# Kernel tuning notes

Hardware: AMD Instinct MI355X
Metric: run time of the kernel (lower is better)

## Reference

```python
import jax, jax.numpy as jnp
import numpy as np
from jax import lax

EPS_LN = 1e-5
EPS_NORM = 1e-12

def conv1x1(x, w):
    # x: [b,c,h,w], w: [o,c]
    return jnp.einsum('oc,bchw->bohw', w, x)

def dwconv3x3(x, w):
    # depthwise 3x3, w: [c,1,3,3]
    return lax.conv_general_dilated(
        x, w, window_strides=(1, 1), padding=[(1, 1), (1, 1)],
        feature_group_count=x.shape[1],
        dimension_numbers=('NCHW', 'OIHW', 'NCHW'))

def layernorm_chan(x, w, b):
    # WithBias LayerNorm over channel dim of NCHW (torch does it in b,(hw),c layout)
    mu = jnp.mean(x, axis=1, keepdims=True)
    var = jnp.mean((x - mu) ** 2, axis=1, keepdims=True)
    xn = (x - mu) / jnp.sqrt(var + EPS_LN)
    return xn * w[None, :, None, None] + b[None, :, None, None]

def l2norm(x):
    n = jnp.sqrt(jnp.sum(x * x, axis=-1, keepdims=True))
    return x / jnp.maximum(n, EPS_NORM)

def setup_inputs() -> dict:
    key = jax.random.key(0)
    ks = jax.random.split(key, 8)
    dim, heads, hidden = 64, 2, 170
    b, h, w = 2, 256, 256
    s = 0.05
    return {
        'x': jax.random.normal(ks[0], (b, dim, h, w), jnp.float32),
        'ln1_w': jnp.ones((dim,), jnp.float32),
        'ln1_b': jnp.zeros((dim,), jnp.float32),
        'w_qkv': jax.random.normal(ks[1], (dim * 3, dim), jnp.float32) * s,
        'dw_qkv': jax.random.normal(ks[2], (dim * 3, 1, 3, 3), jnp.float32) * s,
        'temperature': jnp.ones((heads, 1, 1), jnp.float32),
        'w_po': jax.random.normal(ks[3], (dim, dim), jnp.float32) * s,
        'ln2_w': jnp.ones((dim,), jnp.float32),
        'ln2_b': jnp.zeros((dim,), jnp.float32),
        'w_in': jax.random.normal(ks[4], (hidden * 2, dim), jnp.float32) * s,
        'dw_ffn': jax.random.normal(ks[5], (hidden * 2, 1, 3, 3), jnp.float32) * s,
        'w_out': jax.random.normal(ks[6], (dim, hidden), jnp.float32) * s,
    }

def attention(x, w_qkv, dw_qkv, temperature, w_po, num_heads):
    b, c, h, w = x.shape
    qkv = dwconv3x3(conv1x1(x, w_qkv), dw_qkv)            # [b,3c,h,w]
    q, k, v = jnp.split(qkv, 3, axis=1)
    def heads(t):
        return t.reshape(b, num_heads, c // num_heads, h * w)  # [b,hd,ch,hw]
    q, k, v = heads(q), heads(k), heads(v)
    q = l2norm(q)
    k = l2norm(k)
    attn = jnp.einsum('bhcs,bhds->bhcd', q, k) * temperature[None]  # [b,hd,ch,ch]
    attn = jax.nn.softmax(attn, axis=-1)
    out = jnp.einsum('bhcd,bhds->bhcs', attn, v)
    out = out.reshape(b, c, h, w)
    return conv1x1(out, w_po)

def gdfn(x, w_in, dw_ffn, w_out):
    x = dwconv3x3(conv1x1(x, w_in), dw_ffn)
    x1, x2 = jnp.split(x, 2, axis=1)
    return conv1x1(jax.nn.gelu(x1, approximate=False) * x2, w_out)

def reference(x, ln1_w, ln1_b, w_qkv, dw_qkv, temperature, w_po,
              ln2_w, ln2_b, w_in, dw_ffn, w_out):
    num_heads = temperature.shape[0]
    x = x + attention(layernorm_chan(x, ln1_w, ln1_b), w_qkv, dw_qkv,
                      temperature, w_po, num_heads)
    x = x + gdfn(layernorm_chan(x, ln2_w, ln2_b), w_in, dw_ffn, w_out)
    return x
```

## Files before the change

### kernel.cpp

```cpp
#include <hip/hip_runtime.h>
#include <math.h>

#define HW 65536

typedef __attribute__((ext_vector_type(8))) short short8;
typedef __attribute__((ext_vector_type(4))) float floatx4;
typedef __attribute__((ext_vector_type(4))) unsigned short ushortx4;

__device__ __forceinline__ float bf2f(unsigned short u){
  unsigned v = ((unsigned)u)<<16; float f; __builtin_memcpy(&f,&v,4); return f;
}
__device__ __forceinline__ unsigned short f2bf(float f){
  unsigned u; __builtin_memcpy(&u,&f,4);
  u += 0x7fffu + ((u>>16)&1u);
  return (unsigned short)(u>>16);
}
__device__ __forceinline__ int is_f32(const void* magic){
  return ((const unsigned*)magic)[0] == 0x3F800000u;
}
__device__ __forceinline__ float ldv(const void* p, size_t i, int f32){
  return f32 ? ((const float*)p)[i] : bf2f(((const unsigned short*)p)[i]);
}

__global__ __launch_bounds__(64) void k_fold(const void* __restrict__ w_qkv,
                       const void* __restrict__ ln1_w,
                       const void* __restrict__ ln1_b,
                       const void* __restrict__ w_in,
                       const void* __restrict__ ln2_w,
                       const void* __restrict__ ln2_b,
                       const void* __restrict__ w_out,
                       unsigned short* __restrict__ A1, float* __restrict__ a1, float* __restrict__ b1,
                       unsigned short* __restrict__ A5, float* __restrict__ a5, float* __restrict__ b5,
                       unsigned short* __restrict__ A7){
  int f32 = is_f32(ln1_w);
  int bid = blockIdx.x; int c = threadIdx.x;
  if (bid < 192){
    int j = bid;
    float wv = ldv(w_qkv, j*64+c, f32);
    unsigned short q = f2bf(wv*ldv(ln1_w,c,f32));
    A1[j*64+c] = q;
    float sa = bf2f(q);
    float sb = wv*ldv(ln1_b,c,f32);
    #pragma unroll
    for(int o=1;o<64;o<<=1){ sa += __shfl_xor(sa,o,64); sb += __shfl_xor(sb,o,64); }
    if (c==0){ a1[j]=sa; b1[j]=sb; }
  } else if (bid < 576){
    int j = bid-192;
    float wv = (j<340)? ldv(w_in, j*64+c, f32) : 0.f;
    unsigned short q = f2bf(wv*ldv(ln2_w,c,f32));
    A5[j*64+c]=q;
    float sa = bf2f(q);
    float sb = wv*ldv(ln2_b,c,f32);
    #pragma unroll
    for(int o=1;o<64;o<<=1){ sa += __shfl_xor(sa,o,64); sb += __shfl_xor(sb,o,64); }
    if (c==0){ a5[j]=sa; b5[j]=sb; }
  } else {
    int j = bid-576;
    #pragma unroll
    for(int t=0;t<3;t++){
      int k=t*64+c;
      A7[j*192+k] = (k<170)? f2bf(ldv(w_out, j*170+k, f32)) : (unsigned short)0;
    }
  }
}

#define BTT_STR 72
template<int F32>
__device__ __forceinline__ void gemm_ln_body(
    const unsigned short* __restrict__ A, const void* __restrict__ Bv,
    const float* __restrict__ arow, const float* __restrict__ brow,
    unsigned short* __restrict__ out, int outC, int jmax, int ntiles)
{
  __shared__ unsigned short btt[64*BTT_STR];
  __shared__ float muL[64];
  __shared__ float rsL[64];
  int tid=threadIdx.x; int w=tid>>6, lane=tid&63, m=lane&15, quad=lane>>4;
  int sblk = blockIdx.x*64; int b=sblk>>16, s=sblk&65535;
  {
    int ch = lane, px0 = w*16;
    size_t src = (size_t)b*64*HW + (size_t)ch*HW + s + px0;
    unsigned short tmp[16];
    if (F32){
      const float* sp = (const float*)Bv + src;
      #pragma unroll
      for(int q4=0;q4<4;q4++){
        floatx4 fv = *(const floatx4*)(sp + q4*4);
        #pragma unroll
        for(int k=0;k<4;k++) tmp[q4*4+k] = f2bf(fv[k]);
      }
    } else {
      const unsigned short* sp = (const unsigned short*)Bv + src;
      short8 r0 = *(const short8*)sp;
      short8 r1 = *(const short8*)(sp+8);
      #pragma unroll
      for(int jj=0;jj<8;jj++){ tmp[jj]=(unsigned short)r0[jj]; tmp[8+jj]=(unsigned short)r1[jj]; }
    }
    #pragma unroll
    for(int jj=0;jj<16;jj++) btt[(px0+jj)*BTT_STR + ch] = tmp[jj];
  }
  __syncthreads();
  short8 bfr[4][2];
  #pragma unroll
  for(int st4=0; st4<4; st4++){
    const unsigned short* row = btt + (st4*16+m)*BTT_STR + quad*8;
    short8 v0 = *(const short8*)row;
    short8 v1 = *(const short8*)(row+32);
    bfr[st4][0]=v0; bfr[st4][1]=v1;
    float sm=0.f, sq=0.f;
    #pragma unroll
    for(int jj=0;jj<8;jj++){
      float a=bf2f((unsigned short)v0[jj]); sm+=a; sq+=a*a;
      float c=bf2f((unsigned short)v1[jj]); sm+=c; sq+=c*c;
    }
    sm += __shfl_xor(sm,16,64); sq += __shfl_xor(sq,16,64);
    sm += __shfl_xor(sm,32,64); sq += __shfl_xor(sq,32,64);
    float m_ = sm*(1.f/64.f);
    float var = sq*(1.f/64.f) - m_*m_;
    if (w==0 && quad==0){ muL[st4*16+m]=m_; rsL[st4*16+m]=1.f/sqrtf(var+1e-5f); }
  }
  __syncthreads();
  for(int jt=w; jt<ntiles; jt+=4){
    int j = jt*16 + m;
    const unsigned short* ap = A + j*64 + quad*8;
    short8 af0 = *(const short8*)ap;
    short8 af1 = *(const short8*)(ap+32);
    float aj = arow[j], bj = brow[j];
    unsigned short* op = out + ((size_t)b*outC + j)*HW + s;
    bool ok = (j < jmax);
    #pragma unroll
    for(int st4=0; st4<4; st4++){
      floatx4 acc = {0.f,0.f,0.f,0.f};
      acc = __builtin_amdgcn_mfma_f32_16x16x32_bf16(bfr[st4][0], af0, acc, 0,0,0);
      acc = __builtin_amdgcn_mfma_f32_16x16x32_bf16(bfr[st4][1], af1, acc, 0,0,0);
      floatx4 m4 = *(const floatx4*)(muL + st4*16 + quad*4);
      floatx4 r4 = *(const floatx4*)(rsL + st4*16 + quad*4);
      ushortx4 pk;
      #pragma unroll
      for(int r=0;r<4;r++) pk[r] = f2bf(r4[r]*(acc[r] - m4[r]*aj) + bj);
      if (ok) *(ushortx4*)(op + st4*16 + quad*4) = pk;
    }
  }
}
__global__ __launch_bounds__(256) void k_gemm_ln(
    const unsigned short* __restrict__ A, const void* __restrict__ B,
    const float* __restrict__ arow, const float* __restrict__ brow,
    unsigned short* __restrict__ out,
    int outC, int jmax, int ntiles, const void* __restrict__ magic, int mode)
{
  int f32 = (mode==1) ? 1 : (mode==2 ? 0 : is_f32(magic));
  if (f32) gemm_ln_body<1>(A,B,arow,brow,out,outC,jmax,ntiles);
  else     gemm_ln_body<0>(A,B,arow,brow,out,outC,jmax,ntiles);
}

#define GTT_STR 200
__global__ __launch_bounds__(256) void k_gemm_out(
    const unsigned short* __restrict__ A7, const unsigned short* __restrict__ G,
    const unsigned short* __restrict__ xmid, void* __restrict__ outp, const void* __restrict__ magic)
{
  __shared__ unsigned short gtt[64*GTT_STR];
  int f32 = is_f32(magic);
  int tid=threadIdx.x; int w=tid>>6, lane=tid&63, m=lane&15, quad=lane>>4;
  int sblk = blockIdx.x*64; int b=sblk>>16, s=sblk&65535;
  const unsigned short* Gb = G + (size_t)b*170*HW + s;
  {
    int px0 = w*16;
    #pragma unroll
    for(int rep=0; rep<3; rep++){
      int ch = rep*64 + lane;
      const unsigned short* sp = Gb + (size_t)ch*HW + px0;
      short8 r0 = *(const short8*)sp;
      short8 r1 = *(const short8*)(sp+8);
      #pragma unroll
      for(int jj=0;jj<8;jj++){
        gtt[(px0+jj)*GTT_STR + ch]   = (unsigned short)r0[jj];
        gtt[(px0+8+jj)*GTT_STR + ch] = (unsigned short)r1[jj];
      }
    }
  }
  __syncthreads();
  int j = w*16 + m;
  const unsigned short* ap = A7 + j*192 + quad*8;
  short8 af[6];
  #pragma unroll
  for(int ks=0;ks<6;ks++) af[ks] = *(const short8*)(ap + ks*32);
  #pragma unroll
  for(int st4=0; st4<4; st4++){
    const unsigned short* row = gtt + (st4*16+m)*GTT_STR + quad*8;
    floatx4 acc = {0.f,0.f,0.f,0.f};
    #pragma unroll
    for(int ks=0;ks<6;ks++){
      short8 bf = *(const short8*)(row + ks*32);
      acc = __builtin_amdgcn_mfma_f32_16x16x32_bf16(bf, af[ks], acc, 0,0,0);
    }
    size_t idx0 = ((size_t)b*64 + j)*HW + s + st4*16 + quad*4;
    ushortx4 xm4 = *(const ushortx4*)(xmid + idx0);
    if (f32){
      floatx4 o;
      #pragma unroll
      for(int r=0;r<4;r++) o[r] = acc[r] + bf2f(xm4[r]);
      *(floatx4*)((float*)outp + idx0) = o;
    } else {
      ushortx4 o;
      #pragma unroll
      for(int r=0;r<4;r++) o[r] = f2bf(acc[r] + bf2f(xm4[r]));
      *(ushortx4*)((unsigned short*)outp + idx0) = o;
    }
  }
}

#define TSTRIDE 72
#define TROWS 66
#define TDW 34

__device__ __forceinline__ void stage_tile(unsigned short* __restrict__ tile,
    const unsigned short* __restrict__ sp, int y0, int x0, int tid){
  int ly = tid/TDW, dc = tid - ly*TDW;
  for(int i=tid; i<TROWS*TDW; i+=256){
    int gy = y0+ly-1, gx = x0+2*dc-2;
    unsigned v = 0;
    if((unsigned)gy<256u && (unsigned)gx<256u)
      v = *(const unsigned*)(sp + gy*256 + gx);
    *(unsigned*)(tile + ly*TSTRIDE + 2*dc) = v;
    ly += 7; dc += 18; if(dc>=TDW){dc-=TDW; ly++;}
  }
}

__device__ __forceinline__ void stage_tile2(unsigned short* __restrict__ t1,
    unsigned short* __restrict__ t2,
    const unsigned short* __restrict__ s1, const unsigned short* __restrict__ s2,
    int y0, int x0, int tid){
  int ly = tid/TDW, dc = tid - ly*TDW;
  for(int i=tid; i<TROWS*TDW; i+=256){
    int gy = y0+ly-1, gx = x0+2*dc-2;
    unsigned v1 = 0, v2 = 0;
    if((unsigned)gy<256u && (unsigned)gx<256u){
      int o = gy*256+gx;
      v1 = *(const unsigned*)(s1 + o);
      v2 = *(const unsigned*)(s2 + o);
    }
    *(unsigned*)(t1 + ly*TSTRIDE + 2*dc) = v1;
    *(unsigned*)(t2 + ly*TSTRIDE + 2*dc) = v2;
    ly += 7; dc += 18; if(dc>=TDW){dc-=TDW; ly++;}
  }
}

__device__ __forceinline__ void row_window(const unsigned short* __restrict__ tile,
    int ly, int tx, float* __restrict__ f){
  short8 v0 = *(const short8*)(tile + ly*TSTRIDE + 8*tx);
  short8 v1 = *(const short8*)(tile + ly*TSTRIDE + 8*tx + 8);
  #pragma unroll
  for(int k=0;k<8;k++){ f[k]=bf2f((unsigned short)v0[k]); f[k+8]=bf2f((unsigned short)v1[k]); }
}

__global__ __launch_bounds__(256) void k_dwconv(const unsigned short* __restrict__ src,
    const void* __restrict__ wdw, unsigned short* __restrict__ dst, int C,
    const void* __restrict__ magic){
  int f32 = is_f32(magic);
  __shared__ unsigned short tile[TROWS*TSTRIDE];
  int tid=threadIdx.x;
  int bc = blockIdx.y;
  int ch = bc % C;
  int t = blockIdx.x; int ty0=t>>2, tx0=t&3;
  int y0=ty0*64, x0=tx0*64;
  const unsigned short* sp = src + (size_t)bc*HW;
  stage_tile(tile, sp, y0, x0, tid);
  float w9[9];
  #pragma unroll
  for(int i=0;i<9;i++) w9[i]=ldv(wdw, ch*9+i, f32);
  __syncthreads();
  int tx=tid&7, ty=tid>>3;
  float acc0[8], acc1[8];
  #pragma unroll
  for(int i=0;i<8;i++){ acc0[i]=0.f; acc1[i]=0.f; }
  #pragma unroll
  for(int r=0;r<4;r++){
    int ly = 2*ty + r;
    float f[16];
    row_window(tile, ly, tx, f);
    #pragma unroll
    for(int yy=0;yy<2;yy++){
      int dy = r-yy;
      if (dy>=0 && dy<3){
        float* acc = yy? acc1 : acc0;
        #pragma unroll
        for(int i=0;i<8;i++)
          #pragma unroll
          for(int dx=0;dx<3;dx++)
            acc[i] += w9[dy*3+dx]*f[i+1+dx];
      }
    }
  }
  unsigned short* dp = dst + (size_t)bc*HW + (size_t)(y0+2*ty)*256 + x0 + 8*tx;
  short8 st0, st1;
  #pragma unroll
  for(int i=0;i<8;i++){ st0[i]=(short)f2bf(acc0[i]); st1[i]=(short)f2bf(acc1[i]); }
  *(short8*)dp = st0;
  *(short8*)(dp+256) = st1;
}

__global__ __launch_bounds__(256) void k_ffn_dw(const unsigned short* __restrict__ src,
    const void* __restrict__ wdw, unsigned short* __restrict__ g,
    const void* __restrict__ magic){
  int f32 = is_f32(magic);
  __shared__ unsigned short t1[TROWS*TSTRIDE];
  __shared__ unsigned short t2[TROWS*TSTRIDE];
  int tid=threadIdx.x;
  int bi = blockIdx.y;
  int b = bi/170, i = bi - b*170;
  int t = blockIdx.x; int ty0=t>>2, tx0=t&3;
  int y0=ty0*64, x0=tx0*64;
  const unsigned short* s1 = src + ((size_t)b*340 + i)*HW;
  const unsigned short* s2 = src + ((size_t)b*340 + 170 + i)*HW;
  stage_tile2(t1, t2, s1, s2, y0, x0, tid);
  float wa[9], wb[9];
  #pragma unroll
  for(int q=0;q<9;q++){ wa[q]=ldv(wdw, i*9+q, f32); wb[q]=ldv(wdw, (i+170)*9+q, f32); }
  __syncthreads();
  int tx=tid&7, ty=tid>>3;
  float a0[8], a1v[8], c0[8], c1[8];
  #pragma unroll
  for(int k=0;k<8;k++){ a0[k]=0.f; a1v[k]=0.f; c0[k]=0.f; c1[k]=0.f; }
  #pragma unroll
  for(int r=0;r<4;r++){
    int ly = 2*ty + r;
    float f[16];
    row_window(t1, ly, tx, f);
    #pragma unroll
    for(int yy=0;yy<2;yy++){
      int dy = r-yy;
      if (dy>=0 && dy<3){
        float* acc = yy? a1v : a0;
        #pragma unroll
        for(int k=0;k<8;k++)
          #pragma unroll
          for(int dx=0;dx<3;dx++)
            acc[k] += wa[dy*3+dx]*f[k+1+dx];
      }
    }
    row_window(t2, ly, tx, f);
    #pragma unroll
    for(int yy=0;yy<2;yy++){
      int dy = r-yy;
      if (dy>=0 && dy<3){
        float* acc = yy? c1 : c0;
        #pragma unroll
        for(int k=0;k<8;k++)
          #pragma unroll
          for(int dx=0;dx<3;dx++)
            acc[k] += wb[dy*3+dx]*f[k+1+dx];
      }
    }
  }
  unsigned short* gp = g + ((size_t)b*170 + i)*HW + (size_t)(y0+2*ty)*256 + x0 + 8*tx;
  short8 st0, st1;
  #pragma unroll
  for(int k=0;k<8;k++){
    float u0 = a0[k]*(1.59576912f + 0.07135481f*a0[k]*a0[k]);
    float u1 = a1v[k]*(1.59576912f + 0.07135481f*a1v[k]*a1v[k]);
    float ge0 = a0[k]/(1.f + __expf(-u0));
    float ge1 = a1v[k]/(1.f + __expf(-u1));
    st0[k]=(short)f2bf(ge0*c0[k]);
    st1[k]=(short)f2bf(ge1*c1[k]);
  }
  *(short8*)gp = st0;
  *(short8*)(gp+256) = st1;
}

__global__ __launch_bounds__(256) void k_attn_qk(const unsigned short* __restrict__ qkv,
    float* __restrict__ S, float* __restrict__ qn, float* __restrict__ kn){
  int tid=threadIdx.x; int w=tid>>6, lane=tid&63, m=lane&15, quad=lane>>4;
  int ct=w>>1, dt=w&1;
  int bh=blockIdx.y; int b=bh>>1, hd=bh&1;
  int p0 = blockIdx.x*512;
  const unsigned short* qrow = qkv + ((size_t)(b*192 + hd*32 + ct*16 + m))*HW + p0 + quad*8;
  const unsigned short* krow = qkv + ((size_t)(b*192 + 64 + hd*32 + dt*16 + m))*HW + p0 + quad*8;
  floatx4 acc = {0.f,0.f,0.f,0.f};
  float nq=0.f, nk=0.f;
  for(int it=0; it<16; it++){
    short8 a = *(const short8*)(qrow + it*32);
    short8 bq = *(const short8*)(krow + it*32);
    if (dt==0){
      #pragma unroll
      for(int jj=0;jj<8;jj++){ float v=bf2f((unsigned short)a[jj]); nq+=v*v; }
    }
    if (ct==0){
      #pragma unroll
      for(int jj=0;jj<8;jj++){ float v=bf2f((unsigned short)bq[jj]); nk+=v*v; }
    }
    acc = __builtin_amdgcn_mfma_f32_16x16x32_bf16(a, bq, acc, 0,0,0);
  }
  nq += __shfl_xor(nq,16,64); nq += __shfl_xor(nq,32,64);
  nk += __shfl_xor(nk,16,64); nk += __shfl_xor(nk,32,64);
  if (dt==0 && quad==0) atomicAdd(&qn[bh*32 + ct*16 + m], nq);
  if (ct==0 && quad==0) atomicAdd(&kn[bh*32 + dt*16 + m], nk);
  #pragma unroll
  for(int r=0;r<4;r++)
    atomicAdd(&S[(bh*32 + ct*16 + quad*4 + r)*32 + dt*16 + m], acc[r]);
}

__global__ void k_attn_fin(const float* __restrict__ S, const float* __restrict__ qn,
    const float* __restrict__ kn, const void* __restrict__ temp,
    const void* __restrict__ w_po, unsigned short* __restrict__ Mbf,
    const void* __restrict__ magic){
  int f32 = is_f32(magic);
  __shared__ float attn[2][32][32];
  __shared__ float invq[64], invk[64];
  int b = blockIdx.x; int tid=threadIdx.x;
  if (tid<64){
    int bh=b*2+(tid>>5); int c=tid&31;
    invq[tid] = 1.f/fmaxf(sqrtf(qn[bh*32+c]),1e-12f);
    invk[tid] = 1.f/fmaxf(sqrtf(kn[bh*32+c]),1e-12f);
  }
  __syncthreads();
  if (tid<64){
    int hd=tid>>5, c=tid&31; int bh=b*2+hd;
    float tmp = ldv(temp, hd, f32);
    float row[32]; float mx=-1e30f;
    for(int d=0;d<32;d++){
      float v = S[(bh*32+c)*32+d]*invq[tid]*invk[hd*32+d]*tmp;
      row[d]=v; mx=fmaxf(mx,v);
    }
    float sum=0.f;
    for(int d=0;d<32;d++){ row[d]=expf(row[d]-mx); sum+=row[d]; }
    float inv=1.f/sum;
    for(int d=0;d<32;d++) attn[hd][c][d]=row[d]*inv;
  }
  __syncthreads();
  for(int idx=tid; idx<4096; idx+=256){
    int o=idx>>6, d=idx&63; int hd=d>>5, dd=d&31;
    float sacc=0.f;
    for(int c=0;c<32;c++) sacc += ldv(w_po, o*64 + hd*32 + c, f32) * attn[hd][c][dd];
    Mbf[(size_t)b*4096 + o*64 + d] = f2bf(sacc);
  }
}

#define XSTR 72
__global__ __launch_bounds__(256) void k_attn_ffn(const void* __restrict__ x,
    const unsigned short* __restrict__ qkv, const unsigned short* __restrict__ Mbf,
    unsigned short* __restrict__ xmid,
    const unsigned short* __restrict__ A5, const float* __restrict__ a5, const float* __restrict__ b5,
    unsigned short* __restrict__ ffn_pre, const void* __restrict__ magic){
  __shared__ unsigned short vtt[64*XSTR];
  __shared__ unsigned short xt[64*XSTR];
  __shared__ float muL[64];
  __shared__ float rsL[64];
  int f32 = is_f32(magic);
  int tid=threadIdx.x; int w=tid>>6, lane=tid&63, m=lane&15, quad=lane>>4;
  int sblk = blockIdx.x*64; int b=sblk>>16, s=sblk&65535;
  const unsigned short* vp = qkv + ((size_t)(b*192 + 128))*HW + s;
  {
    int ch = lane, px0 = w*16;
    const unsigned short* sp = vp + (size_t)ch*HW + px0;
    short8 r0 = *(const short8*)sp;
    short8 r1 = *(const short8*)(sp+8);
    #pragma unroll
    for(int jj=0;jj<8;jj++){
      vtt[(px0+jj)*XSTR + ch]   = (unsigned short)r0[jj];
      vtt[(px0+8+jj)*XSTR + ch] = (unsigned short)r1[jj];
    }
  }
  int jme = w*16 + m;
  const unsigned short* ap = Mbf + (size_t)b*4096 + jme*64 + quad*8;
  short8 af0 = *(const short8*)ap;
  short8 af1 = *(const short8*)(ap+32);
  __syncthreads();
  short8 bfr[4][2];
  #pragma unroll
  for(int st4=0; st4<4; st4++){
    const unsigned short* row = vtt + (st4*16+m)*XSTR + quad*8;
    bfr[st4][0] = *(const short8*)row;
    bfr[st4][1] = *(const short8*)(row+32);
  }
  size_t xbase = (size_t)b*64*HW + s;
  #pragma unroll
  for(int st4=0; st4<4; st4++){
    floatx4 acc = {0.f,0.f,0.f,0.f};
    acc = __builtin_amdgcn_mfma_f32_16x16x32_bf16(bfr[st4][0], af0, acc, 0,0,0);
    acc = __builtin_amdgcn_mfma_f32_16x16x32_bf16(bfr[st4][1], af1, acc, 0,0,0);
    size_t idx0 = xbase + (size_t)jme*HW + st4*16 + quad*4;
    ushortx4 h;
    if (f32){
      floatx4 x4 = *(const floatx4*)((const float*)x + idx0);
      #pragma unroll
      for(int r=0;r<4;r++) h[r] = f2bf(acc[r] + x4[r]);
    } else {
      ushortx4 x4 = *(const ushortx4*)((const unsigned short*)x + idx0);
      #pragma unroll
      for(int r=0;r<4;r++) h[r] = f2bf(acc[r] + bf2f(x4[r]));
    }
    *(ushortx4*)(xmid + idx0) = h;
    #pragma unroll
    for(int r=0;r<4;r++) xt[(st4*16+quad*4+r)*XSTR + jme] = h[r];
  }
  __syncthreads();
  #pragma unroll
  for(int st4=0; st4<4; st4++){
    const unsigned short* row = xt + (st4*16+m)*XSTR + quad*8;
    short8 v0 = *(const short8*)row;
    short8 v1 = *(const short8*)(row+32);
    bfr[st4][0]=v0; bfr[st4][1]=v1;
    float sm=0.f, sq=0.f;
    #pragma unroll
    for(int jj=0;jj<8;jj++){
      float a=bf2f((unsigned short)v0[jj]); sm+=a; sq+=a*a;
      float c=bf2f((unsigned short)v1[jj]); sm+=c; sq+=c*c;
    }
    sm += __shfl_xor(sm,16,64); sq += __shfl_xor(sq,16,64);
    sm += __shfl_xor(sm,32,64); sq += __shfl_xor(sq,32,64);
    float m_ = sm*(1.f/64.f);
    float var = sq*(1.f/64.f) - m_*m_;
    if (w==0 && quad==0){ muL[st4*16+m]=m_; rsL[st4*16+m]=1.f/sqrtf(var+1e-5f); }
  }
  __syncthreads();
  for(int jt=w; jt<24; jt+=4){
    int j = jt*16 + m;
    const unsigned short* a5p = A5 + j*64 + quad*8;
    short8 g0 = *(const short8*)a5p;
    short8 g1 = *(const short8*)(a5p+32);
    float aj = a5[j], bj = b5[j];
    unsigned short* op = ffn_pre + ((size_t)b*340 + j)*HW + s;
    bool ok = (j < 340);
    #pragma unroll
    for(int st4=0; st4<4; st4++){
      floatx4 acc = {0.f,0.f,0.f,0.f};
      acc = __builtin_amdgcn_mfma_f32_16x16x32_bf16(bfr[st4][0], g0, acc, 0,0,0);
      acc = __builtin_amdgcn_mfma_f32_16x16x32_bf16(bfr[st4][1], g1, acc, 0,0,0);
      floatx4 m4 = *(const floatx4*)(muL + st4*16 + quad*4);
      floatx4 r4 = *(const floatx4*)(rsL + st4*16 + quad*4);
      ushortx4 pk;
      #pragma unroll
      for(int r=0;r<4;r++) pk[r] = f2bf(r4[r]*(acc[r] - m4[r]*aj) + bj);
      if (ok) *(ushortx4*)(op + st4*16 + quad*4) = pk;
    }
  }
}

extern "C" void kernel_launch(void* const* d_in, const int* in_sizes, int n_in,
                              void* d_out, int out_size, void* d_ws, size_t ws_size,
                              hipStream_t stream){
  (void)in_sizes; (void)n_in; (void)out_size; (void)ws_size;
  const void* x     = d_in[0];
  const void* ln1_w = d_in[1];
  const void* ln1_b = d_in[2];
  const void* w_qkv = d_in[3];
  const void* dw_qkv= d_in[4];
  const void* temp  = d_in[5];
  const void* w_po  = d_in[6];
  const void* ln2_w = d_in[7];
  const void* ln2_b = d_in[8];
  const void* w_in  = d_in[9];
  const void* dw_ffn= d_in[10];
  const void* w_out = d_in[11];

  char* ws = (char*)d_ws;
  size_t off = 0;
  auto alloc = [&](size_t n)->void*{ void* p = ws + off; off = (off + n + 255) & ~(size_t)255; return p; };

  unsigned short* A1 = (unsigned short*)alloc(192*64*2);
  float* a1 = (float*)alloc(192*4);
  float* b1 = (float*)alloc(192*4);
  unsigned short* A5 = (unsigned short*)alloc(384*64*2);
  float* a5 = (float*)alloc(384*4);
  float* b5 = (float*)alloc(384*4);
  unsigned short* A7 = (unsigned short*)alloc(64*192*2);
  float* S  = (float*)alloc(4*32*32*4);
  float* qn = (float*)alloc(128*4);
  float* kn = (float*)alloc(128*4);
  unsigned short* Mbf = (unsigned short*)alloc(2*64*64*2);
  unsigned short* xmid = (unsigned short*)alloc((size_t)2*64*HW*2);
  unsigned short* regionA = (unsigned short*)alloc((size_t)2*340*HW*2);
  unsigned short* regionB = (unsigned short*)alloc((size_t)2*192*HW*2);

  k_fold<<<dim3(640), dim3(64), 0, stream>>>(w_qkv, ln1_w, ln1_b, w_in, ln2_w, ln2_b, w_out,
                                             A1, a1, b1, A5, a5, b5, A7);

  k_gemm_ln<<<dim3(2048), dim3(256), 0, stream>>>(A1, x, a1, b1, regionA, 192, 192, 12, ln1_w, 0);
  k_dwconv<<<dim3(16,384), dim3(256), 0, stream>>>(regionA, dw_qkv, regionB, 192, ln1_w);

  hipMemsetAsync(S, 0, 16384+512+512, stream);
  k_attn_qk<<<dim3(128,4), dim3(256), 0, stream>>>(regionB, S, qn, kn);
  k_attn_fin<<<dim3(2), dim3(256), 0, stream>>>(S, qn, kn, temp, w_po, Mbf, ln1_w);

  k_attn_ffn<<<dim3(2048), dim3(256), 0, stream>>>(x, regionB, Mbf, xmid,
                                                   A5, a5, b5, regionA, ln1_w);
  k_ffn_dw<<<dim3(16,340), dim3(256), 0, stream>>>(regionA, dw_ffn, regionB, ln1_w);
  k_gemm_out<<<dim3(2048), dim3(256), 0, stream>>>(A7, regionB, xmid, d_out, ln1_w);
}
```

Measured before the change: 312.5 us.

## Replace LDS-tiled depthwise convs with register rolling-row column strips

Both depthwise 3x3 kernels drop the shared-memory halo tile and barrier. Each thread now owns an 8-pixel column strip of 16 rows and loads rows straight from global memory into a rotating 4-row register window, with halo pixels fetched as scalar loads. The grid shrinks from 16 to 2 blocks per channel. This removes LDS staging and the sync and cuts the vertical halo overhead. In exchange it adds unaligned scalar edge loads, a longer serial dependency per thread, and fewer blocks in flight.

```diff
diff --git a/kernel.cpp b/kernel.cpp
--- a/kernel.cpp
+++ b/kernel.cpp
@@ -208,162 +208,112 @@
   }
 }
 
-#define TSTRIDE 72
-#define TROWS 66
-#define TDW 34
-
-__device__ __forceinline__ void stage_tile(unsigned short* __restrict__ tile,
-    const unsigned short* __restrict__ sp, int y0, int x0, int tid){
-  int ly = tid/TDW, dc = tid - ly*TDW;
-  for(int i=tid; i<TROWS*TDW; i+=256){
-    int gy = y0+ly-1, gx = x0+2*dc-2;
-    unsigned v = 0;
-    if((unsigned)gy<256u && (unsigned)gx<256u)
-      v = *(const unsigned*)(sp + gy*256 + gx);
-    *(unsigned*)(tile + ly*TSTRIDE + 2*dc) = v;
-    ly += 7; dc += 18; if(dc>=TDW){dc-=TDW; ly++;}
-  }
-}
-
-__device__ __forceinline__ void stage_tile2(unsigned short* __restrict__ t1,
-    unsigned short* __restrict__ t2,
-    const unsigned short* __restrict__ s1, const unsigned short* __restrict__ s2,
-    int y0, int x0, int tid){
-  int ly = tid/TDW, dc = tid - ly*TDW;
-  for(int i=tid; i<TROWS*TDW; i+=256){
-    int gy = y0+ly-1, gx = x0+2*dc-2;
-    unsigned v1 = 0, v2 = 0;
-    if((unsigned)gy<256u && (unsigned)gx<256u){
-      int o = gy*256+gx;
-      v1 = *(const unsigned*)(s1 + o);
-      v2 = *(const unsigned*)(s2 + o);
-    }
-    *(unsigned*)(t1 + ly*TSTRIDE + 2*dc) = v1;
-    *(unsigned*)(t2 + ly*TSTRIDE + 2*dc) = v2;
-    ly += 7; dc += 18; if(dc>=TDW){dc-=TDW; ly++;}
-  }
-}
-
-__device__ __forceinline__ void row_window(const unsigned short* __restrict__ tile,
-    int ly, int tx, float* __restrict__ f){
-  short8 v0 = *(const short8*)(tile + ly*TSTRIDE + 8*tx);
-  short8 v1 = *(const short8*)(tile + ly*TSTRIDE + 8*tx + 8);
-  #pragma unroll
-  for(int k=0;k<8;k++){ f[k]=bf2f((unsigned short)v0[k]); f[k+8]=bf2f((unsigned short)v1[k]); }
+__device__ __forceinline__ void load_row(const unsigned short* __restrict__ sp,
+    int y, int x0, int oct, float* __restrict__ f){
+  if((unsigned)y < 256u){
+    const unsigned short* p = sp + y*256 + x0;
+    short8 v = *(const short8*)p;
+    #pragma unroll
+    for(int k=0;k<8;k++) f[k+1] = bf2f((unsigned short)v[k]);
+    f[0] = oct      ? bf2f(p[-1]) : 0.f;
+    f[9] = (oct<31) ? bf2f(p[8])  : 0.f;
+  } else {
+    #pragma unroll
+    for(int k=0;k<10;k++) f[k] = 0.f;
+  }
+}
+
+__device__ __forceinline__ void conv_row(const float* __restrict__ r0,
+    const float* __restrict__ r1, const float* __restrict__ r2,
+    const float* __restrict__ w, float* __restrict__ o){
+  #pragma unroll
+  for(int k=0;k<8;k++){
+    o[k] = w[0]*r0[k] + w[1]*r0[k+1] + w[2]*r0[k+2]
+         + w[3]*r1[k] + w[4]*r1[k+1] + w[5]*r1[k+2]
+         + w[6]*r2[k] + w[7]*r2[k+1] + w[8]*r2[k+2];
+  }
 }
 
 __global__ __launch_bounds__(256) void k_dwconv(const unsigned short* __restrict__ src,
     const void* __restrict__ wdw, unsigned short* __restrict__ dst, int C,
     const void* __restrict__ magic){
   int f32 = is_f32(magic);
-  __shared__ unsigned short tile[TROWS*TSTRIDE];
   int tid=threadIdx.x;
   int bc = blockIdx.y;
   int ch = bc % C;
-  int t = blockIdx.x; int ty0=t>>2, tx0=t&3;
-  int y0=ty0*64, x0=tx0*64;
+  int oct = tid&31, strip = tid>>5;
+  int x0 = oct*8;
+  int y0 = blockIdx.x*128 + strip*16;
   const unsigned short* sp = src + (size_t)bc*HW;
-  stage_tile(tile, sp, y0, x0, tid);
   float w9[9];
   #pragma unroll
   for(int i=0;i<9;i++) w9[i]=ldv(wdw, ch*9+i, f32);
-  __syncthreads();
-  int tx=tid&7, ty=tid>>3;
-  float acc0[8], acc1[8];
-  #pragma unroll
-  for(int i=0;i<8;i++){ acc0[i]=0.f; acc1[i]=0.f; }
-  #pragma unroll
-  for(int r=0;r<4;r++){
-    int ly = 2*ty + r;
-    float f[16];
-    row_window(tile, ly, tx, f);
-    #pragma unroll
-    for(int yy=0;yy<2;yy++){
-      int dy = r-yy;
-      if (dy>=0 && dy<3){
-        float* acc = yy? acc1 : acc0;
-        #pragma unroll
-        for(int i=0;i<8;i++)
-          #pragma unroll
-          for(int dx=0;dx<3;dx++)
-            acc[i] += w9[dy*3+dx]*f[i+1+dx];
-      }
-    }
-  }
-  unsigned short* dp = dst + (size_t)bc*HW + (size_t)(y0+2*ty)*256 + x0 + 8*tx;
-  short8 st0, st1;
-  #pragma unroll
-  for(int i=0;i<8;i++){ st0[i]=(short)f2bf(acc0[i]); st1[i]=(short)f2bf(acc1[i]); }
-  *(short8*)dp = st0;
-  *(short8*)(dp+256) = st1;
+  unsigned short* dp = dst + (size_t)bc*HW + (size_t)y0*256 + x0;
+  float A[10],B[10],C_[10],D[10];
+  load_row(sp, y0-1, x0, oct, A);
+  load_row(sp, y0,   x0, oct, B);
+  load_row(sp, y0+1, x0, oct, C_);
+  int y = y0;
+#define DSTEP(P,Q,R,S) { \
+    load_row(sp, y+2, x0, oct, S); \
+    float o8[8]; \
+    conv_row(P,Q,R, w9, o8); \
+    short8 st; \
+    _Pragma("unroll") \
+    for(int k=0;k<8;k++) st[k]=(short)f2bf(o8[k]); \
+    *(short8*)dp = st; dp += 256; y++; }
+  for(int t=0;t<4;t++){
+    DSTEP(A,B,C_,D)
+    DSTEP(B,C_,D,A)
+    DSTEP(C_,D,A,B)
+    DSTEP(D,A,B,C_)
+  }
+#undef DSTEP
 }
 
 __global__ __launch_bounds__(256) void k_ffn_dw(const unsigned short* __restrict__ src,
     const void* __restrict__ wdw, unsigned short* __restrict__ g,
     const void* __restrict__ magic){
   int f32 = is_f32(magic);
-  __shared__ unsigned short t1[TROWS*TSTRIDE];
-  __shared__ unsigned short t2[TROWS*TSTRIDE];
   int tid=threadIdx.x;
   int bi = blockIdx.y;
   int b = bi/170, i = bi - b*170;
-  int t = blockIdx.x; int ty0=t>>2, tx0=t&3;
-  int y0=ty0*64, x0=tx0*64;
+  int oct = tid&31, strip = tid>>5;
+  int x0 = oct*8;
+  int y0 = blockIdx.x*128 + strip*16;
   const unsigned short* s1 = src + ((size_t)b*340 + i)*HW;
   const unsigned short* s2 = src + ((size_t)b*340 + 170 + i)*HW;
-  stage_tile2(t1, t2, s1, s2, y0, x0, tid);
   float wa[9], wb[9];
   #pragma unroll
   for(int q=0;q<9;q++){ wa[q]=ldv(wdw, i*9+q, f32); wb[q]=ldv(wdw, (i+170)*9+q, f32); }
-  __syncthreads();
-  int tx=tid&7, ty=tid>>3;
-  float a0[8], a1v[8], c0[8], c1[8];
-  #pragma unroll
-  for(int k=0;k<8;k++){ a0[k]=0.f; a1v[k]=0.f; c0[k]=0.f; c1[k]=0.f; }
-  #pragma unroll
-  for(int r=0;r<4;r++){
-    int ly = 2*ty + r;
-    float f[16];
-    row_window(t1, ly, tx, f);
-    #pragma unroll
-    for(int yy=0;yy<2;yy++){
-      int dy = r-yy;
-      if (dy>=0 && dy<3){
-        float* acc = yy? a1v : a0;
-        #pragma unroll
-        for(int k=0;k<8;k++)
-          #pragma unroll
-          for(int dx=0;dx<3;dx++)
-            acc[k] += wa[dy*3+dx]*f[k+1+dx];
-      }
-    }
-    row_window(t2, ly, tx, f);
-    #pragma unroll
-    for(int yy=0;yy<2;yy++){
-      int dy = r-yy;
-      if (dy>=0 && dy<3){
-        float* acc = yy? c1 : c0;
-        #pragma unroll
-        for(int k=0;k<8;k++)
-          #pragma unroll
-          for(int dx=0;dx<3;dx++)
-            acc[k] += wb[dy*3+dx]*f[k+1+dx];
-      }
-    }
-  }
-  unsigned short* gp = g + ((size_t)b*170 + i)*HW + (size_t)(y0+2*ty)*256 + x0 + 8*tx;
-  short8 st0, st1;
-  #pragma unroll
-  for(int k=0;k<8;k++){
-    float u0 = a0[k]*(1.59576912f + 0.07135481f*a0[k]*a0[k]);
-    float u1 = a1v[k]*(1.59576912f + 0.07135481f*a1v[k]*a1v[k]);
-    float ge0 = a0[k]/(1.f + __expf(-u0));
-    float ge1 = a1v[k]/(1.f + __expf(-u1));
-    st0[k]=(short)f2bf(ge0*c0[k]);
-    st1[k]=(short)f2bf(ge1*c1[k]);
-  }
-  *(short8*)gp = st0;
-  *(short8*)(gp+256) = st1;
+  unsigned short* gp = g + ((size_t)b*170 + i)*HW + (size_t)y0*256 + x0;
+  float A1[10],B1[10],C1[10],D1[10];
+  float A2[10],B2[10],C2[10],D2[10];
+  load_row(s1, y0-1, x0, oct, A1); load_row(s2, y0-1, x0, oct, A2);
+  load_row(s1, y0,   x0, oct, B1); load_row(s2, y0,   x0, oct, B2);
+  load_row(s1, y0+1, x0, oct, C1); load_row(s2, y0+1, x0, oct, C2);
+  int y = y0;
+#define FSTEP(P,Q,R,S) { \
+    load_row(s1, y+2, x0, oct, S##1); \
+    load_row(s2, y+2, x0, oct, S##2); \
+    float oa[8], oc[8]; \
+    conv_row(P##1,Q##1,R##1, wa, oa); \
+    conv_row(P##2,Q##2,R##2, wb, oc); \
+    short8 st; \
+    _Pragma("unroll") \
+    for(int k=0;k<8;k++){ \
+      float u = oa[k]*(1.59576912f + 0.07135481f*oa[k]*oa[k]); \
+      float ge = oa[k]/(1.f + __expf(-u)); \
+      st[k]=(short)f2bf(ge*oc[k]); \
+    } \
+    *(short8*)gp = st; gp += 256; y++; }
+  for(int t=0;t<4;t++){
+    FSTEP(A,B,C,D)
+    FSTEP(B,C,D,A)
+    FSTEP(C,D,A,B)
+    FSTEP(D,A,B,C)
+  }
+#undef FSTEP
 }
 
 __global__ __launch_bounds__(256) void k_attn_qk(const unsigned short* __restrict__ qkv,
@@ -575,7 +525,7 @@
                                              A1, a1, b1, A5, a5, b5, A7);
 
   k_gemm_ln<<<dim3(2048), dim3(256), 0, stream>>>(A1, x, a1, b1, regionA, 192, 192, 12, ln1_w, 0);
-  k_dwconv<<<dim3(16,384), dim3(256), 0, stream>>>(regionA, dw_qkv, regionB, 192, ln1_w);
+  k_dwconv<<<dim3(2,384), dim3(256), 0, stream>>>(regionA, dw_qkv, regionB, 192, ln1_w);
 
   hipMemsetAsync(S, 0, 16384+512+512, stream);
   k_attn_qk<<<dim3(128,4), dim3(256), 0, stream>>>(regionB, S, qn, kn);
@@ -583,6 +533,6 @@
 
   k_attn_ffn<<<dim3(2048), dim3(256), 0, stream>>>(x, regionB, Mbf, xmid,
                                                    A5, a5, b5, regionA, ln1_w);
-  k_ffn_dw<<<dim3(16,340), dim3(256), 0, stream>>>(regionA, dw_ffn, regionB, ln1_w);
+  k_ffn_dw<<<dim3(2,340), dim3(256), 0, stream>>>(regionA, dw_ffn, regionB, ln1_w);
   k_gemm_out<<<dim3(2048), dim3(256), 0, stream>>>(A7, regionB, xmid, d_out, ln1_w);
 }
```

Measured after the change: 308.6 us. No clear change (-1.3%).
